# Performance work log

Measured on AMD Instinct MI355X. Metric: run time of the kernel, lower is better.

Reference implementation:

```python
import jax, jax.numpy as jnp
import numpy as np

NEG_INF = -jnp.inf


def setup_inputs() -> dict:
    B, T, E, H = 16, 1024, 1024, 1024  # batch, seq, embed_dim, head_dim (T <= H required by original buffer slicing)
    key = jax.random.key(0)
    k1, k2, k3, k4, k5, k6 = jax.random.split(key, 6)
    return {
        "key": jax.random.normal(k1, (B, T, E), dtype=jnp.float32),
        "query": jax.random.normal(k2, (B, T, E), dtype=jnp.float32),
        "value": jax.random.normal(k3, (B, T, E), dtype=jnp.float32),
        "padding_mask": jnp.zeros((B, 1, T), dtype=jnp.int32),
        # nn.Linear(embed_dim, head_dim, bias=False) weights: [head_dim, embed_dim]
        "Wk": jax.random.normal(k4, (H, E), dtype=jnp.float32) * (E ** -0.5),
        "Wq": jax.random.normal(k5, (H, E), dtype=jnp.float32) * (E ** -0.5),
        "Wv": jax.random.normal(k6, (H, E), dtype=jnp.float32) * (E ** -0.5),
    }


def reference(key, query, value, padding_mask, Wk, Wq, Wv):
    # key/query/value: [B, T, E]; W*: [H, E]
    B, T, E = key.shape
    k = jnp.einsum("bte,he->bth", key, Wk)
    q = jnp.einsum("bte,he->bth", query, Wq)
    v = jnp.einsum("bte,he->bth", value, Wv)
    # NOTE: original scales by d_k = key.size(-1) = embed_dim, not head_dim
    scale = 1.0 / jnp.sqrt(jnp.float32(E))
    qk = jnp.einsum("bth,bsh->bts", q, k) * scale  # [B, T, T]
    # causal buffer is tril(ones, diagonal=1): position i can attend to j <= i+1
    causal = jnp.tril(jnp.ones((T, T), dtype=jnp.float32), k=1)
    qk = jnp.where(causal == 0, NEG_INF, qk)
    qk = jnp.where(padding_mask == 1, NEG_INF, qk)  # padding_mask broadcasts [B,1,T] -> [B,T,T]
    p = jax.nn.softmax(qk, axis=-1)
    attn = jnp.einsum("bts,bsh->bth", p, v)  # dropout is identity in eval mode
    return attn
```

## Files before the change

### kernel.cpp

```cpp
#include <hip/hip_runtime.h>
#include <hip/hip_bf16.h>
#include <stdint.h>

typedef __bf16 bf16;
typedef __attribute__((ext_vector_type(8))) __bf16 bf16x8;
typedef __attribute__((ext_vector_type(4))) __bf16 bf16x4;
typedef __attribute__((ext_vector_type(4))) float  f32x4;

static __device__ __forceinline__ void gll16(const void* g, void* lds_base) {
  __builtin_amdgcn_global_load_lds((__attribute__((address_space(1))) void*)g,
                                   (__attribute__((address_space(3))) void*)lds_base,
                                   16, 0, 0);
}

#define BARR  __builtin_amdgcn_s_barrier()
#define VMW(N) asm volatile("s_waitcnt vmcnt(" #N ")" ::: "memory")
#define LGKM0 asm volatile("s_waitcnt lgkmcnt(0)" ::: "memory")
#define SB0   __builtin_amdgcn_sched_barrier(0)

template <int VARIANT>
__global__ __launch_bounds__(512, 2) void gemm8(const bf16* __restrict__ a0,
                                                const bf16* __restrict__ a1,
                                                const bf16* __restrict__ b0,
                                                const bf16* __restrict__ b1,
                                                bf16* __restrict__ c0,
                                                bf16* __restrict__ c1,
                                                float* __restrict__ Cf,
                                                const int* __restrict__ pad) {
  extern __shared__ char smem[];
  char* ldsA = smem;
  char* ldsB = smem + 32768;

  const int tid = threadIdx.x;
  const int lane = tid & 63, wave = tid >> 6;
  const int lo = lane & 15, hi = lane >> 4;
  const int wmi = wave >> 2, wni = wave & 3;
  const int swz = ((lo >> 1) & 3) << 4;

  const int nwg = gridDim.x;
  const int id = (blockIdx.x % 8) * (nwg >> 3) + blockIdx.x / 8;

  int row0, col0, nt, batch = 0, trans = 0;
  const bf16 *Ap, *Bp;
  bf16* Cb;
  if (VARIANT == 0) {
    const int seg = id >> 8, idl = id & 255;
    row0 = (idl >> 2) * 256; col0 = (idl & 3) * 256; nt = 32;
    trans = seg;
    const bf16* As = seg ? a1 : a0;
    const bf16* Bs = seg ? b1 : b0;
    Cb = seg ? c1 : c0;
    Ap = As + (size_t)row0 * 1024;
    Bp = Bs + (size_t)col0 * 1024;
  } else {
    batch = id >> 4;
    const int r = id & 15, it = r >> 2, jt = r & 3;
    row0 = it * 256; col0 = jt * 256;
    nt = (VARIANT == 3) ? min(32, 8 * it + 10) : 32;
    if (VARIANT == 2 && jt > it + 1) return;
    if (VARIANT == 2 && jt == it + 1) {
      bf16* Sb = c0 + ((size_t)batch << 20);
      bf16x8 z = {};
#pragma unroll
      for (int q = 0; q < 16; ++q) {
        const int off = (q * 512 + tid) * 8;
        *(bf16x8*)(Sb + (size_t)(row0 + (off >> 8)) * 1024 + col0 + (off & 255)) = z;
      }
      return;
    }
    Ap = a0 + ((size_t)batch << 20) + (size_t)row0 * 1024;
    Bp = b0 + ((size_t)batch << 20) + (size_t)col0 * 1024;
    Cb = c0;
  }
  const int ntm1 = nt - 1;

  auto stg = [&](const bf16* base, char* ldsOp, int tidx, int slot) {
    const int tc = tidx > ntm1 ? ntm1 : tidx;
#pragma unroll
    for (int r = 0; r < 2; ++r) {
      const int x  = wave * 2048 + r * 1024 + lane * 16;
      const int xs = x ^ (((x >> 7) & 3) << 4);
      gll16((const char*)base + (size_t)(xs >> 6) * 2048 + (size_t)tc * 64 + (xs & 63),
            ldsOp + slot * 16384 + wave * 2048 + r * 1024);
    }
  };

  f32x4 acc[8][4] = {};
  bf16x8 af[4], bfr[4];

  auto rdA = [&](int mh, int slot) {
#pragma unroll
    for (int i = 0; i < 4; ++i) {
      const int row = wmi * 128 + mh * 64 + i * 16 + lo;
      af[i] = *(const bf16x8*)(ldsA + slot * 16384 + ((row * 64 + hi * 16) ^ swz));
    }
  };
  auto rdB = [&](int slot) {
#pragma unroll
    for (int n = 0; n < 4; ++n) {
      const int row = wni * 64 + n * 16 + lo;
      bfr[n] = *(const bf16x8*)(ldsB + slot * 16384 + ((row * 64 + hi * 16) ^ swz));
    }
  };
  auto mmaQ = [&](int mh) {
    __builtin_amdgcn_s_setprio(1);
#pragma unroll
    for (int i = 0; i < 4; ++i)
#pragma unroll
      for (int n = 0; n < 4; ++n)
        acc[mh * 4 + i][n] = __builtin_amdgcn_mfma_f32_16x16x32_bf16(
            af[i], bfr[n], acc[mh * 4 + i][n], 0, 0, 0);
    __builtin_amdgcn_s_setprio(0);
  };

  stg(Bp, ldsB, 0, 0);
  stg(Ap, ldsA, 0, 0);
  stg(Bp, ldsB, 1, 1);
  VMW(2);
  BARR;

#pragma unroll 2
  for (int u = 0; u < nt; ++u) {
    const int cur = u & 1;
    rdA(0, cur);
    rdB(cur);
    stg(Ap, ldsA, u + 1, cur ^ 1);
    BARR; LGKM0; SB0;
    mmaQ(0);
    BARR;
    rdA(1, cur);
    stg(Bp, ldsB, u + 2, cur);
    BARR; LGKM0; SB0;
    mmaQ(1);
    VMW(2);
    BARR;
  }

  if (VARIANT == 0) {
    if (!trans) {
#pragma unroll
      for (int m = 0; m < 8; ++m)
#pragma unroll
        for (int n = 0; n < 4; ++n) {
          const int c = col0 + wni * 64 + n * 16 + lo;
          const int rbase = row0 + wmi * 128 + m * 16 + hi * 4;
#pragma unroll
          for (int j = 0; j < 4; ++j)
            Cb[(size_t)(rbase + j) * 1024 + c] = (bf16)acc[m][n][j];
        }
    } else {
#pragma unroll
      for (int m = 0; m < 8; ++m)
#pragma unroll
        for (int n = 0; n < 4; ++n) {
          const int r = row0 + wmi * 128 + m * 16 + hi * 4;
          const int c = col0 + wni * 64 + n * 16 + lo;
          const int bb = r >> 10, tt = r & 1023;
          bf16x4 h = { (bf16)acc[m][n][0], (bf16)acc[m][n][1],
                       (bf16)acc[m][n][2], (bf16)acc[m][n][3] };
          *(bf16x4*)(Cb + ((size_t)bb << 20) + ((size_t)c << 10) + tt) = h;
        }
    }
  } else if (VARIANT == 2) {
    const float NINF = -__builtin_inff();
#pragma unroll
    for (int n = 0; n < 4; ++n) {
      const int s = col0 + wni * 64 + n * 16 + lo;
      const int pd = pad[(batch << 10) + s];
#pragma unroll
      for (int m = 0; m < 8; ++m) {
        const int tbase = row0 + wmi * 128 + m * 16 + hi * 4;
#pragma unroll
        for (int j = 0; j < 4; ++j) {
          float v = acc[m][n][j] * 0.03125f;
          if (s > tbase + j + 1) v = 0.f;
          else if (pd != 0) v = NINF;
          Cb[((size_t)batch << 20) + (size_t)(tbase + j) * 1024 + s] = (bf16)v;
        }
      }
    }
  } else {
#pragma unroll
    for (int m = 0; m < 8; ++m)
#pragma unroll
      for (int n = 0; n < 4; ++n) {
        const int h2 = col0 + wni * 64 + n * 16 + lo;
        const int tbase = row0 + wmi * 128 + m * 16 + hi * 4;
#pragma unroll
        for (int j = 0; j < 4; ++j)
          Cf[((size_t)batch << 20) + (size_t)(tbase + j) * 1024 + h2] = acc[m][n][j];
      }
  }
  asm volatile("s_waitcnt vmcnt(0)" ::: "memory");
}

__global__ __launch_bounds__(256) void cvt3_kernel(const float* __restrict__ s0,
                                                   const float* __restrict__ s1,
                                                   const float* __restrict__ s2,
                                                   bf16* __restrict__ d0,
                                                   bf16* __restrict__ d1,
                                                   bf16* __restrict__ d2) {
  const int seg = blockIdx.x >> 13, blk = blockIdx.x & 8191;
  const float* src = seg == 0 ? s0 : (seg == 1 ? s1 : s2);
  bf16* dst = seg == 0 ? d0 : (seg == 1 ? d1 : d2);
  const int i = (blk * 256 + threadIdx.x) * 8;
  const f32x4 a = *(const f32x4*)(src + i);
  const f32x4 b = *(const f32x4*)(src + i + 4);
  bf16x8 o = { (bf16)a[0], (bf16)a[1], (bf16)a[2], (bf16)a[3],
               (bf16)b[0], (bf16)b[1], (bf16)b[2], (bf16)b[3] };
  *(bf16x8*)(dst + i) = o;
}

__global__ __launch_bounds__(256) void cvtWT_kernel(const float* __restrict__ Wq,
                                                    const float* __restrict__ Wk,
                                                    const float* __restrict__ Wv,
                                                    bf16* __restrict__ WqT,
                                                    bf16* __restrict__ WkT,
                                                    bf16* __restrict__ Wvb) {
  const int t = threadIdx.x;
  if (blockIdx.x >= 512) {
    const int i = ((blockIdx.x - 512) * 256 + t) * 8;
    const f32x4 a = *(const f32x4*)(Wv + i);
    const f32x4 b = *(const f32x4*)(Wv + i + 4);
    bf16x8 o = { (bf16)a[0], (bf16)a[1], (bf16)a[2], (bf16)a[3],
                 (bf16)b[0], (bf16)b[1], (bf16)b[2], (bf16)b[3] };
    *(bf16x8*)(Wvb + i) = o;
    return;
  }
  const int m = blockIdx.x >> 8;
  const float* src = m ? Wk : Wq;
  bf16* dst = m ? WkT : WqT;
  const int tile = blockIdx.x & 255;
  const int tr = (tile >> 4) * 64, tc = (tile & 15) * 64;
  __shared__ bf16 s[64][72];
#pragma unroll
  for (int it = 0; it < 4; ++it) {
    const int row = it * 16 + (t >> 4), col = (t & 15) * 4;
    const f32x4 v = *(const f32x4*)(src + (size_t)(tr + row) * 1024 + tc + col);
#pragma unroll
    for (int j = 0; j < 4; ++j) s[col + j][row] = (bf16)v[j];
  }
  __syncthreads();
  const int c = t >> 2, rb = (t & 3) * 16;
  bf16* d = dst + (size_t)(tc + c) * 1024 + tr + rb;
  *(bf16x8*)(d)     = *(const bf16x8*)&s[c][rb];
  *(bf16x8*)(d + 8) = *(const bf16x8*)&s[c][rb + 8];
}

__global__ __launch_bounds__(64) void corner_kernel(const bf16* __restrict__ Y,
                                                    const bf16* __restrict__ Xk,
                                                    const int* __restrict__ pad,
                                                    bf16* __restrict__ S) {
  const int b = blockIdx.x / 3, it = blockIdx.x % 3;
  const int t = it * 256 + 255, s = (it + 1) * 256;
  const int lane = threadIdx.x;
  const bf16* y = Y  + ((size_t)b << 20) + (size_t)t * 1024 + lane * 16;
  const bf16* k = Xk + ((size_t)b << 20) + (size_t)s * 1024 + lane * 16;
  bf16x8 q0 = *(const bf16x8*)y, q1 = *(const bf16x8*)(y + 8);
  bf16x8 k0 = *(const bf16x8*)k, k1 = *(const bf16x8*)(k + 8);
  float d = 0.f;
#pragma unroll
  for (int j = 0; j < 8; ++j) d += (float)q0[j] * (float)k0[j] + (float)q1[j] * (float)k1[j];
#pragma unroll
  for (int o = 32; o; o >>= 1) d += __shfl_xor(d, o, 64);
  if (lane == 0) {
    float v = d * 0.03125f;
    if (pad[(b << 10) + s] != 0) v = -__builtin_inff();
    S[((size_t)b << 20) + (size_t)t * 1024 + s] = (bf16)v;
  }
}

__global__ __launch_bounds__(256) void softmax_kernel(bf16* __restrict__ S) {
  const int row  = blockIdx.x * 4 + (threadIdx.x >> 6);
  const int lane = threadIdx.x & 63;
  const int t = row & 1023;
  const int w = min(1024, t + 2);
  const bool act = lane * 16 < w;
  bf16* r = S + (size_t)row * 1024 + lane * 16;
  bf16x8 v0 = {}, v1 = {};
  float f[16];
#pragma unroll
  for (int j = 0; j < 16; ++j) f[j] = -1e30f;
  if (act) {
    v0 = *(const bf16x8*)r;
    v1 = *(const bf16x8*)(r + 8);
#pragma unroll
    for (int j = 0; j < 16; ++j)
      if (lane * 16 + j < w) f[j] = (float)(j < 8 ? v0[j] : v1[j - 8]);
  }
  float m = f[0];
#pragma unroll
  for (int j = 1; j < 16; ++j) m = fmaxf(m, f[j]);
#pragma unroll
  for (int o = 32; o; o >>= 1) m = fmaxf(m, __shfl_xor(m, o, 64));
  float sum = 0.f;
  float e[16];
#pragma unroll
  for (int j = 0; j < 16; ++j) { e[j] = __expf(f[j] - m); sum += e[j]; }
#pragma unroll
  for (int o = 32; o; o >>= 1) sum += __shfl_xor(sum, o, 64);
  const float inv = 1.0f / sum;
  if (act) {
#pragma unroll
    for (int j = 0; j < 8; ++j) {
      v0[j] = (bf16)(lane * 16 + j < w ? e[j] * inv : 0.f);
      v1[j] = (bf16)(lane * 16 + 8 + j < w ? e[8 + j] * inv : 0.f);
    }
    *(bf16x8*)r = v0;
    *(bf16x8*)(r + 8) = v1;
  }
}

extern "C" void kernel_launch(void* const* d_in, const int* in_sizes, int n_in,
                              void* d_out, int out_size, void* d_ws, size_t ws_size,
                              hipStream_t stream) {
  const float* key   = (const float*)d_in[0];
  const float* query = (const float*)d_in[1];
  const float* value = (const float*)d_in[2];
  const int*   pad   = (const int*)d_in[3];
  const float* Wk    = (const float*)d_in[4];
  const float* Wq    = (const float*)d_in[5];
  const float* Wv    = (const float*)d_in[6];
  float* out = (float*)d_out;

  bf16* WqT = (bf16*)d_ws;
  bf16* WkT = WqT + (1 << 20);
  bf16* Wvb = WkT + (1 << 20);
  bf16* P   = Wvb + (1 << 20);
  bf16* Y   = P   + (1 << 20);
  bf16* vT  = Y   + (16 << 20);
  bf16* S   = vT  + (16 << 20);
  bf16* Xq  = S;
  bf16* Xk  = (bf16*)d_out;
  bf16* Xv  = Xk + (16 << 20);

  hipFuncSetAttribute(reinterpret_cast<const void*>(&gemm8<0>),
                      hipFuncAttributeMaxDynamicSharedMemorySize, 65536);
  hipFuncSetAttribute(reinterpret_cast<const void*>(&gemm8<2>),
                      hipFuncAttributeMaxDynamicSharedMemorySize, 65536);
  hipFuncSetAttribute(reinterpret_cast<const void*>(&gemm8<3>),
                      hipFuncAttributeMaxDynamicSharedMemorySize, 65536);

  cvtWT_kernel<<<1024, 256, 0, stream>>>(Wq, Wk, Wv, WqT, WkT, Wvb);
  gemm8<0><<<16, 512, 65536, stream>>>(WkT, nullptr, WqT, nullptr,
                                       P, nullptr, nullptr, nullptr);
  cvt3_kernel<<<24576, 256, 0, stream>>>(query, key, value, Xq, Xk, Xv);

  gemm8<0><<<512, 512, 65536, stream>>>(Xq, Xv, P, Wvb, Y, vT, nullptr, nullptr);

  gemm8<2><<<256, 512, 65536, stream>>>(Y, nullptr, Xk, nullptr,
                                        S, nullptr, nullptr, pad);
  corner_kernel<<<48, 64, 0, stream>>>(Y, Xk, pad, S);
  softmax_kernel<<<4096, 256, 0, stream>>>(S);
  gemm8<3><<<256, 512, 65536, stream>>>(S, nullptr, vT, nullptr,
                                        nullptr, nullptr, out, nullptr);
}
```

Baseline: 238.1 us.

## Use 128-row tiles for QK and PV GEMMs to skip more causal work

The attention-score and PV GEMM variants move from 256x256 to 128x256 tiles, doubling the grid to 512 blocks and shrinking LDS to 48KB. The finer row granularity lets the causal mask skip more tiles, and zero-fill now covers tiles whose first column is at least row0+256. The PV K-loop bound follows the finer rows. The separate corner kernel for the diagonal+1 element is removed, since the tile boundaries now fall so the QK GEMM computes that element. The trade-off is less operand reuse per tile and more blocks.

Result: no change. 240.5 us (+1.0%).

```diff
diff --git a/kernel.cpp b/kernel.cpp
--- a/kernel.cpp
+++ b/kernel.cpp
@@ -27,9 +27,13 @@
                                                 bf16* __restrict__ c1,
                                                 float* __restrict__ Cf,
                                                 const int* __restrict__ pad) {
+  constexpr int TM = (VARIANT == 0) ? 256 : 128;
+  constexpr int ABYTES = TM * 64;
+  constexpr int AROUNDS = ABYTES / 8192;
+  constexpr int FI = TM / 64;
   extern __shared__ char smem[];
   char* ldsA = smem;
-  char* ldsB = smem + 32768;
+  char* ldsB = smem + 2 * ABYTES;
 
   const int tid = threadIdx.x;
   const int lane = tid & 63, wave = tid >> 6;
@@ -53,16 +57,15 @@
     Ap = As + (size_t)row0 * 1024;
     Bp = Bs + (size_t)col0 * 1024;
   } else {
-    batch = id >> 4;
-    const int r = id & 15, it = r >> 2, jt = r & 3;
-    row0 = it * 256; col0 = jt * 256;
-    nt = (VARIANT == 3) ? min(32, 8 * it + 10) : 32;
-    if (VARIANT == 2 && jt > it + 1) return;
-    if (VARIANT == 2 && jt == it + 1) {
+    batch = id >> 5;
+    const int it = (id >> 2) & 7, jt = id & 3;
+    row0 = it * 128; col0 = jt * 256;
+    nt = (VARIANT == 3) ? min(32, 4 * it + 5) : 32;
+    if (VARIANT == 2 && 2 * jt >= it + 2) {
       bf16* Sb = c0 + ((size_t)batch << 20);
       bf16x8 z = {};
 #pragma unroll
-      for (int q = 0; q < 16; ++q) {
+      for (int q = 0; q < (TM * 256) / (512 * 8); ++q) {
         const int off = (q * 512 + tid) * 8;
         *(bf16x8*)(Sb + (size_t)(row0 + (off >> 8)) * 1024 + col0 + (off & 255)) = z;
       }
@@ -74,25 +77,35 @@
   }
   const int ntm1 = nt - 1;
 
-  auto stg = [&](const bf16* base, char* ldsOp, int tidx, int slot) {
+  auto stgA = [&](int tidx, int slot) {
     const int tc = tidx > ntm1 ? ntm1 : tidx;
 #pragma unroll
+    for (int r = 0; r < AROUNDS; ++r) {
+      const int x  = (r * 512 + tid) * 16;
+      const int xs = x ^ (((x >> 7) & 3) << 4);
+      gll16((const char*)Ap + (size_t)(xs >> 6) * 2048 + (size_t)tc * 64 + (xs & 63),
+            ldsA + slot * ABYTES + r * 8192 + wave * 1024);
+    }
+  };
+  auto stgB = [&](int tidx, int slot) {
+    const int tc = tidx > ntm1 ? ntm1 : tidx;
+#pragma unroll
     for (int r = 0; r < 2; ++r) {
-      const int x  = wave * 2048 + r * 1024 + lane * 16;
+      const int x  = (r * 512 + tid) * 16;
       const int xs = x ^ (((x >> 7) & 3) << 4);
-      gll16((const char*)base + (size_t)(xs >> 6) * 2048 + (size_t)tc * 64 + (xs & 63),
-            ldsOp + slot * 16384 + wave * 2048 + r * 1024);
-    }
-  };
-
-  f32x4 acc[8][4] = {};
-  bf16x8 af[4], bfr[4];
+      gll16((const char*)Bp + (size_t)(xs >> 6) * 2048 + (size_t)tc * 64 + (xs & 63),
+            ldsB + slot * 16384 + r * 8192 + wave * 1024);
+    }
+  };
+
+  f32x4 acc[2 * FI][4] = {};
+  bf16x8 af[FI], bfr[4];
 
   auto rdA = [&](int mh, int slot) {
 #pragma unroll
-    for (int i = 0; i < 4; ++i) {
-      const int row = wmi * 128 + mh * 64 + i * 16 + lo;
-      af[i] = *(const bf16x8*)(ldsA + slot * 16384 + ((row * 64 + hi * 16) ^ swz));
+    for (int i = 0; i < FI; ++i) {
+      const int row = wmi * (TM / 2) + mh * (TM / 4) + i * 16 + lo;
+      af[i] = *(const bf16x8*)(ldsA + slot * ABYTES + ((row * 64 + hi * 16) ^ swz));
     }
   };
   auto rdB = [&](int slot) {
@@ -105,17 +118,17 @@
   auto mmaQ = [&](int mh) {
     __builtin_amdgcn_s_setprio(1);
 #pragma unroll
-    for (int i = 0; i < 4; ++i)
+    for (int i = 0; i < FI; ++i)
 #pragma unroll
       for (int n = 0; n < 4; ++n)
-        acc[mh * 4 + i][n] = __builtin_amdgcn_mfma_f32_16x16x32_bf16(
-            af[i], bfr[n], acc[mh * 4 + i][n], 0, 0, 0);
+        acc[mh * FI + i][n] = __builtin_amdgcn_mfma_f32_16x16x32_bf16(
+            af[i], bfr[n], acc[mh * FI + i][n], 0, 0, 0);
     __builtin_amdgcn_s_setprio(0);
   };
 
-  stg(Bp, ldsB, 0, 0);
-  stg(Ap, ldsA, 0, 0);
-  stg(Bp, ldsB, 1, 1);
+  stgB(0, 0);
+  stgA(0, 0);
+  stgB(1, 1);
   VMW(2);
   BARR;
 
@@ -124,12 +137,12 @@
     const int cur = u & 1;
     rdA(0, cur);
     rdB(cur);
-    stg(Ap, ldsA, u + 1, cur ^ 1);
+    stgA(u + 1, cur ^ 1);
     BARR; LGKM0; SB0;
     mmaQ(0);
     BARR;
     rdA(1, cur);
-    stg(Bp, ldsB, u + 2, cur);
+    stgB(u + 2, cur);
     BARR; LGKM0; SB0;
     mmaQ(1);
     VMW(2);
@@ -139,21 +152,21 @@
   if (VARIANT == 0) {
     if (!trans) {
 #pragma unroll
-      for (int m = 0; m < 8; ++m)
+      for (int m = 0; m < 2 * FI; ++m)
 #pragma unroll
         for (int n = 0; n < 4; ++n) {
           const int c = col0 + wni * 64 + n * 16 + lo;
-          const int rbase = row0 + wmi * 128 + m * 16 + hi * 4;
+          const int rbase = row0 + wmi * (TM / 2) + m * 16 + hi * 4;
 #pragma unroll
           for (int j = 0; j < 4; ++j)
             Cb[(size_t)(rbase + j) * 1024 + c] = (bf16)acc[m][n][j];
         }
     } else {
 #pragma unroll
-      for (int m = 0; m < 8; ++m)
+      for (int m = 0; m < 2 * FI; ++m)
 #pragma unroll
         for (int n = 0; n < 4; ++n) {
-          const int r = row0 + wmi * 128 + m * 16 + hi * 4;
+          const int r = row0 + wmi * (TM / 2) + m * 16 + hi * 4;
           const int c = col0 + wni * 64 + n * 16 + lo;
           const int bb = r >> 10, tt = r & 1023;
           bf16x4 h = { (bf16)acc[m][n][0], (bf16)acc[m][n][1],
@@ -168,8 +181,8 @@
       const int s = col0 + wni * 64 + n * 16 + lo;
       const int pd = pad[(batch << 10) + s];
 #pragma unroll
-      for (int m = 0; m < 8; ++m) {
-        const int tbase = row0 + wmi * 128 + m * 16 + hi * 4;
+      for (int m = 0; m < 2 * FI; ++m) {
+        const int tbase = row0 + wmi * (TM / 2) + m * 16 + hi * 4;
 #pragma unroll
         for (int j = 0; j < 4; ++j) {
           float v = acc[m][n][j] * 0.03125f;
@@ -181,11 +194,11 @@
     }
   } else {
 #pragma unroll
-    for (int m = 0; m < 8; ++m)
+    for (int m = 0; m < 2 * FI; ++m)
 #pragma unroll
       for (int n = 0; n < 4; ++n) {
         const int h2 = col0 + wni * 64 + n * 16 + lo;
-        const int tbase = row0 + wmi * 128 + m * 16 + hi * 4;
+        const int tbase = row0 + wmi * (TM / 2) + m * 16 + hi * 4;
 #pragma unroll
         for (int j = 0; j < 4; ++j)
           Cf[((size_t)batch << 20) + (size_t)(tbase + j) * 1024 + h2] = acc[m][n][j];
@@ -247,29 +260,6 @@
   *(bf16x8*)(d + 8) = *(const bf16x8*)&s[c][rb + 8];
 }
 
-__global__ __launch_bounds__(64) void corner_kernel(const bf16* __restrict__ Y,
-                                                    const bf16* __restrict__ Xk,
-                                                    const int* __restrict__ pad,
-                                                    bf16* __restrict__ S) {
-  const int b = blockIdx.x / 3, it = blockIdx.x % 3;
-  const int t = it * 256 + 255, s = (it + 1) * 256;
-  const int lane = threadIdx.x;
-  const bf16* y = Y  + ((size_t)b << 20) + (size_t)t * 1024 + lane * 16;
-  const bf16* k = Xk + ((size_t)b << 20) + (size_t)s * 1024 + lane * 16;
-  bf16x8 q0 = *(const bf16x8*)y, q1 = *(const bf16x8*)(y + 8);
-  bf16x8 k0 = *(const bf16x8*)k, k1 = *(const bf16x8*)(k + 8);
-  float d = 0.f;
-#pragma unroll
-  for (int j = 0; j < 8; ++j) d += (float)q0[j] * (float)k0[j] + (float)q1[j] * (float)k1[j];
-#pragma unroll
-  for (int o = 32; o; o >>= 1) d += __shfl_xor(d, o, 64);
-  if (lane == 0) {
-    float v = d * 0.03125f;
-    if (pad[(b << 10) + s] != 0) v = -__builtin_inff();
-    S[((size_t)b << 20) + (size_t)t * 1024 + s] = (bf16)v;
-  }
-}
-
 __global__ __launch_bounds__(256) void softmax_kernel(bf16* __restrict__ S) {
   const int row  = blockIdx.x * 4 + (threadIdx.x >> 6);
   const int lane = threadIdx.x & 63;
@@ -337,9 +327,9 @@
   hipFuncSetAttribute(reinterpret_cast<const void*>(&gemm8<0>),
                       hipFuncAttributeMaxDynamicSharedMemorySize, 65536);
   hipFuncSetAttribute(reinterpret_cast<const void*>(&gemm8<2>),
-                      hipFuncAttributeMaxDynamicSharedMemorySize, 65536);
+                      hipFuncAttributeMaxDynamicSharedMemorySize, 49152);
   hipFuncSetAttribute(reinterpret_cast<const void*>(&gemm8<3>),
-                      hipFuncAttributeMaxDynamicSharedMemorySize, 65536);
+                      hipFuncAttributeMaxDynamicSharedMemorySize, 49152);
 
   cvtWT_kernel<<<1024, 256, 0, stream>>>(Wq, Wk, Wv, WqT, WkT, Wvb);
   gemm8<0><<<16, 512, 65536, stream>>>(WkT, nullptr, WqT, nullptr,
@@ -348,10 +338,9 @@
 
   gemm8<0><<<512, 512, 65536, stream>>>(Xq, Xv, P, Wvb, Y, vT, nullptr, nullptr);
 
-  gemm8<2><<<256, 512, 65536, stream>>>(Y, nullptr, Xk, nullptr,
+  gemm8<2><<<512, 512, 49152, stream>>>(Y, nullptr, Xk, nullptr,
                                         S, nullptr, nullptr, pad);
-  corner_kernel<<<48, 64, 0, stream>>>(Y, Xk, pad, S);
   softmax_kernel<<<4096, 256, 0, stream>>>(S);
-  gemm8<3><<<256, 512, 65536, stream>>>(S, nullptr, vT, nullptr,
+  gemm8<3><<<512, 512, 49152, stream>>>(S, nullptr, vT, nullptr,
                                         nullptr, nullptr, out, nullptr);
 }
```
